# Performance work log

Measured on AMD Instinct MI355X. Metric: run time of the kernel, lower is better.

Reference implementation:

```python
import jax, jax.numpy as jnp
import numpy as np

B, S, E, H = 2, 1024, 4096, 16
D = E // H          # head_dim = 256
RD = 64             # rotary_dim
# Quantization scales (alpha of the int8 GEMM epilogues)
A_QKV = 1.2e-4      # W8A8B8O8 q/k/v projection output scale
A_QK = 2e-4         # BMM_S8T_S8N_F32T alpha (= q_scale * k_scale)
A_PV = 1.0 / 127.0  # BMM_S8T_S8N_S8T alpha (probs quantized by *127)
A_O = 0.01          # W8A8BFP32OFP32 out_proj alpha


def setup_inputs() -> dict:
    key = jax.random.key(0)
    ks = jax.random.split(key, 9)
    ri = lambda k, shp: jax.random.randint(k, shp, -127, 128).astype(jnp.float32)
    return {
        "hidden_states": ri(ks[0], (B, S, E)),   # int8-valued activations
        "Wq": ri(ks[1], (E, E)),
        "Wk": ri(ks[2], (E, E)),
        "Wv": ri(ks[3], (E, E)),
        "Wo": ri(ks[4], (E, E)),
        "bq": ri(ks[5], (E,)),
        "bk": ri(ks[6], (E,)),
        "bv": ri(ks[7], (E,)),
        "bo": jax.random.normal(ks[8], (E,), dtype=jnp.float32) * 0.02,  # fp32 bias
    }


def _linear_i8(x, W, b, alpha):
    # W8A8B8O8Linear: int8 GEMM, scaled, +int8 bias, round+saturate to int8
    y = alpha * (x @ W.T) + b
    return jnp.clip(jnp.round(y), -128, 127)


def _rotate_every_two(x):
    x1 = x[..., ::2]
    x2 = x[..., 1::2]
    return jnp.stack((-x2, x1), axis=-1).reshape(x.shape)


def _apply_rotary(x, sin, cos):
    # duplicate_interleave == repeat each column twice; broadcast over [B, S, H, rd]
    sin = jnp.repeat(sin, 2, axis=-1)[None, :, None, :]
    cos = jnp.repeat(cos, 2, axis=-1)[None, :, None, :]
    r = x * cos + _rotate_every_two(x) * sin
    # torch: clamp(-128,127).to(int8) -> truncate toward zero
    return jnp.trunc(jnp.clip(r, -128.0, 127.0))


def reference(hidden_states, Wq, Wk, Wv, Wo, bq, bk, bv, bo):
    q = _linear_i8(hidden_states, Wq, bq, A_QKV).reshape(B, S, H, D)
    k = _linear_i8(hidden_states, Wk, bk, A_QKV).reshape(B, S, H, D)
    v = _linear_i8(hidden_states, Wv, bv, A_QKV).reshape(B, S, H, D)
    v = v.transpose(0, 2, 1, 3)  # [B, H, S, D]

    # fixed_pos_embedding over rotary_dim
    inv_freq = 1.0 / (10000.0 ** (jnp.arange(0, RD, 2, dtype=jnp.float32) / RD))
    t = jnp.arange(S, dtype=jnp.float32)
    sinusoid = t[:, None] * inv_freq[None, :]   # [S, RD/2]
    sin, cos = jnp.sin(sinusoid), jnp.cos(sinusoid)

    q = jnp.concatenate([_apply_rotary(q[..., :RD], sin, cos), q[..., RD:]], axis=-1)
    k = jnp.concatenate([_apply_rotary(k[..., :RD], sin, cos), k[..., RD:]], axis=-1)
    q = q.transpose(0, 2, 1, 3)  # [B, H, S, D]
    k = k.transpose(0, 2, 1, 3)

    w = A_QK * jnp.einsum('bhqd,bhkd->bhqk', q, k)
    causal = jnp.tril(jnp.ones((S, S), dtype=bool))[None, None]
    w = jnp.where(causal, w, jnp.finfo(jnp.float32).min)
    w = w / jnp.sqrt(jnp.float32(D))  # scale_attn = sqrt(head_dim)
    p = jnp.round(jax.nn.softmax(w, axis=-1) * 127.0)  # int8-valued probs

    # pv_bmm: int8 probs x int8 values -> scaled, round+saturate to int8
    o = jnp.clip(jnp.round(A_PV * jnp.einsum('bhqk,bhkd->bhqd', p, v)), -128, 127)
    o = o.transpose(0, 2, 1, 3).reshape(B, S, E)  # merge heads

    # out_proj: W8A8BFP32OFP32 -> fp32 output
    return A_O * (o @ Wo.T) + bo
```

## Files before the change

### kernel.cpp

```cpp
#include <hip/hip_runtime.h>
#include <hip/hip_bf16.h>

typedef int int32x4 __attribute__((ext_vector_type(4)));
typedef signed char i8;

#define B_ 2
#define S_ 1024
#define E_ 4096
#define H_ 16
#define D_ 256

#define MFMA_I8(a, b, c) __builtin_amdgcn_mfma_i32_16x16x64_i8((a), (b), (c), 0, 0, 0)

__device__ __forceinline__ int32x4 ld16(const void* p) {
    return *reinterpret_cast<const int32x4*>(p);
}

__device__ __forceinline__ void gload16(const void* g, void* l) {
    __builtin_amdgcn_global_load_lds(
        (const __attribute__((address_space(1))) void*)g,
        (__attribute__((address_space(3))) void*)l, 16, 0, 0);
}

#define WAIT_VM3()  asm volatile("s_waitcnt vmcnt(3)" ::: "memory")
#define WAIT_VM0()  asm volatile("s_waitcnt vmcnt(0)" ::: "memory")
#define COMPILER_FENCE() asm volatile("" ::: "memory")

__device__ __forceinline__ int pack4(float4 f) {
    union { int w; i8 b[4]; } u;
    u.b[0] = (i8)f.x; u.b[1] = (i8)f.y; u.b[2] = (i8)f.z; u.b[3] = (i8)f.w;
    return u.w;
}

__global__ void k_f32_to_i8(const float* __restrict__ src, i8* __restrict__ dst, int n4) {
    int i = blockIdx.x * blockDim.x + threadIdx.x;
    if (i >= n4) return;
    reinterpret_cast<int*>(dst)[i] = pack4(reinterpret_cast<const float4*>(src)[i]);
}

__global__ void k_w_to_i8(const float* __restrict__ w0, const float* __restrict__ w1,
                          const float* __restrict__ w2, const float* __restrict__ w3,
                          i8* __restrict__ d0, i8* __restrict__ d1,
                          i8* __restrict__ d2, i8* __restrict__ d3, int n4) {
    int i = blockIdx.x * blockDim.x + threadIdx.x;
    if (i >= n4) return;
    const float* src = (blockIdx.y == 0) ? w0 : (blockIdx.y == 1) ? w1 : (blockIdx.y == 2) ? w2 : w3;
    i8* dst = (blockIdx.y == 0) ? d0 : (blockIdx.y == 1) ? d1 : (blockIdx.y == 2) ? d2 : d3;
    reinterpret_cast<int*>(dst)[i] = pack4(reinterpret_cast<const float4*>(src)[i]);
}

__global__ void k_sincos(float* __restrict__ sin_t, float* __restrict__ cos_t) {
    int idx = blockIdx.x * blockDim.x + threadIdx.x;
    if (idx >= S_ * 32) return;
    int s = idx >> 5, i = idx & 31;
    float ex = (float)(2 * i) / 64.0f;
    float invf = 1.0f / powf(10000.0f, ex);
    float arg = (float)s * invf;
    sin_t[idx] = (float)sin((double)arg);
    cos_t[idx] = (float)cos((double)arg);
}

template<bool OUT_I8>
__device__ __forceinline__ void gemm_core(
    const i8* __restrict__ X, const i8* __restrict__ W, const float* __restrict__ bias,
    void* __restrict__ out, float alpha, int M, int N, int K, i8* lds)
{
    const int nt = K >> 6;
    const int nwg = (M >> 8) * (N >> 7);
    const int q = nwg >> 3;
    const int lin = blockIdx.x;
    const int wg = (lin & 7) * q + (lin >> 3);
    const int nbm = M >> 8;
    const int m0 = (wg % nbm) * 256, n0 = (wg / nbm) * 128;

    const int tid = threadIdx.x, lane = tid & 63, wave = tid >> 6;
    const int wr = wave >> 1, wc = wave & 1, l4 = lane & 15, lh = lane >> 4;

    const int g4 = lh ^ ((l4 >> 1) & 3);
    const int aoff = (wr * 64 + l4) * 64 + g4 * 16;
    const int boff = 16384 + (wc * 64 + l4) * 64 + g4 * 16;

    const int srow = tid >> 2;
    const int sg = (tid & 3) ^ ((tid >> 3) & 3);
    const i8* Asrc = X + (size_t)(m0 + srow) * K + sg * 16;
    const i8* Bsrc = W + (size_t)(n0 + srow) * K + sg * 16;
    const size_t rstep = (size_t)128 * K;
    const int ldst = wave * 1024;

#define BUF(t_) (lds + ((t_) % 3) * 24576)
#define STAGE(t_) do { int kb_ = (t_) * 64; i8* lb_ = BUF(t_);               \
        gload16(Asrc + kb_,         lb_ + ldst);                             \
        gload16(Asrc + rstep + kb_, lb_ + 8192 + ldst);                      \
        gload16(Bsrc + kb_,         lb_ + 16384 + ldst); } while (0)

    int32x4 acc[4][4];
#pragma unroll
    for (int m = 0; m < 4; ++m)
#pragma unroll
        for (int n = 0; n < 4; ++n) acc[m][n] = int32x4{0, 0, 0, 0};

    STAGE(0);
    STAGE(1);

    for (int t = 0; t < nt; ++t) {
        const i8* Tb = BUF(t);
        if (t + 1 < nt) { WAIT_VM3(); } else { WAIT_VM0(); }
        __builtin_amdgcn_s_barrier();
        COMPILER_FENCE();

        if (t + 2 < nt) STAGE(t + 2);

        int32x4 a0, a1, a2, a3, b0, b1, b2, b3;
        a0 = ld16(Tb + aoff);
        b0 = ld16(Tb + boff);        b1 = ld16(Tb + boff + 1024);
        b2 = ld16(Tb + boff + 2048); b3 = ld16(Tb + boff + 3072);
        a1 = ld16(Tb + aoff + 1024);
        a2 = ld16(Tb + aoff + 2048); a3 = ld16(Tb + aoff + 3072);
        __builtin_amdgcn_s_setprio(1);
        acc[0][0] = MFMA_I8(a0, b0, acc[0][0]);
        acc[0][1] = MFMA_I8(a0, b1, acc[0][1]);
        acc[0][2] = MFMA_I8(a0, b2, acc[0][2]);
        acc[0][3] = MFMA_I8(a0, b3, acc[0][3]);
        acc[1][0] = MFMA_I8(a1, b0, acc[1][0]);
        acc[1][1] = MFMA_I8(a1, b1, acc[1][1]);
        acc[1][2] = MFMA_I8(a1, b2, acc[1][2]);
        acc[1][3] = MFMA_I8(a1, b3, acc[1][3]);
        acc[2][0] = MFMA_I8(a2, b0, acc[2][0]);
        acc[2][1] = MFMA_I8(a2, b1, acc[2][1]);
        acc[2][2] = MFMA_I8(a2, b2, acc[2][2]);
        acc[2][3] = MFMA_I8(a2, b3, acc[2][3]);
        acc[3][0] = MFMA_I8(a3, b0, acc[3][0]);
        acc[3][1] = MFMA_I8(a3, b1, acc[3][1]);
        acc[3][2] = MFMA_I8(a3, b2, acc[3][2]);
        acc[3][3] = MFMA_I8(a3, b3, acc[3][3]);
        __builtin_amdgcn_s_setprio(0);
    }
#undef BUF
#undef STAGE

#pragma unroll
    for (int m = 0; m < 4; ++m)
#pragma unroll
        for (int n = 0; n < 4; ++n)
#pragma unroll
            for (int r = 0; r < 4; ++r) {
                int grow = m0 + wr * 64 + m * 16 + lh * 4 + r;
                int gcol = n0 + wc * 64 + n * 16 + l4;
                float y = alpha * (float)acc[m][n][r] + bias[gcol];
                if (OUT_I8) {
                    float v = rintf(y);
                    v = fminf(fmaxf(v, -128.0f), 127.0f);
                    reinterpret_cast<i8*>(out)[(size_t)grow * N + gcol] = (i8)v;
                } else {
                    reinterpret_cast<float*>(out)[(size_t)grow * N + gcol] = y;
                }
            }
}

__global__ __launch_bounds__(512, 4) void k_gemm_qkv(
    const i8* __restrict__ X,
    const i8* __restrict__ w0, const i8* __restrict__ w1, const i8* __restrict__ w2,
    const float* __restrict__ b0, const float* __restrict__ b1, const float* __restrict__ b2,
    i8* __restrict__ o0, i8* __restrict__ o1, i8* __restrict__ o2,
    float alpha, int M, int N, int K)
{
    __shared__ __align__(16) i8 lds[3 * 24576];
    int z = blockIdx.z;
    const i8* W = (z == 0) ? w0 : (z == 1) ? w1 : w2;
    const float* bias = (z == 0) ? b0 : (z == 1) ? b1 : b2;
    i8* out = (z == 0) ? o0 : (z == 1) ? o1 : o2;
    gemm_core<true>(X, W, bias, out, alpha, M, N, K, lds);
}

__global__ __launch_bounds__(512, 4) void k_gemm_out(
    const i8* __restrict__ X, const i8* __restrict__ W, const float* __restrict__ bias,
    float* __restrict__ out, float alpha, int M, int N, int K)
{
    __shared__ __align__(16) i8 lds[3 * 24576];
    gemm_core<false>(X, W, bias, out, alpha, M, N, K, lds);
}

__global__ void k_rope(const i8* __restrict__ qin, const i8* __restrict__ kin,
                       i8* __restrict__ qout, i8* __restrict__ kout,
                       const float* __restrict__ sin_t, const float* __restrict__ cos_t)
{
    const i8* in = blockIdx.y ? kin : qin;
    i8* outp = blockIdx.y ? kout : qout;
    int row = blockIdx.x * 2 + (threadIdx.x >> 7);
    int i = threadIdx.x & 127;
    int b = row / (S_ * H_);
    int s = (row / H_) % S_;
    int h = row % H_;
    const i8* src = in + (size_t)row * D_ + i * 2;
    i8 x1 = src[0], x2 = src[1];
    i8 o1, o2;
    if (i < 32) {
        float c = cos_t[s * 32 + i], sn = sin_t[s * 32 + i];
        float f1 = (float)x1, f2 = (float)x2;
        float r0 = __fadd_rn(__fmul_rn(f1, c), __fmul_rn(-f2, sn));
        float r1 = __fadd_rn(__fmul_rn(f2, c), __fmul_rn(f1, sn));
        r0 = truncf(fminf(fmaxf(r0, -128.0f), 127.0f));
        r1 = truncf(fminf(fmaxf(r1, -128.0f), 127.0f));
        o1 = (i8)r0; o2 = (i8)r1;
    } else { o1 = x1; o2 = x2; }
    size_t ob = ((size_t)(b * H_ + h) * S_ + s) * D_ + i * 2;
    outp[ob] = o1; outp[ob + 1] = o2;
}

__global__ void k_vtrans(const i8* __restrict__ vin, i8* __restrict__ vout) {
    __shared__ int tile[64][17];
    int bh = blockIdx.z;
    int b = bh >> 4, h = bh & 15;
    int s0 = blockIdx.x * 64, d0 = blockIdx.y * 64;
    int t = threadIdx.x;
    {
        int sr = t >> 2, dq = (t & 3) * 16;
        int32x4 v = ld16(vin + ((size_t)(b * S_ + s0 + sr) * H_ + h) * D_ + d0 + dq);
#pragma unroll
        for (int j = 0; j < 4; ++j) tile[sr][dq / 4 + j] = v[j];
    }
    __syncthreads();
    {
        int dr = t >> 2, sq = (t & 3) * 16;
        union { int32x4 v; i8 b[16]; } u;
        const i8* tb = reinterpret_cast<const i8*>(tile);
#pragma unroll
        for (int j = 0; j < 16; ++j) u.b[j] = tb[(sq + j) * 68 + dr];
        *reinterpret_cast<int32x4*>(vout + ((size_t)bh * D_ + d0 + dr) * S_ + s0 + sq) = u.v;
    }
}

struct AttnShared {
    float slx[4][32];
    float r127[32];
    __align__(16) i8 plds[32][80];
};

__device__ __forceinline__ void attn_chunk(int qc, int bh, int tid,
    const i8* __restrict__ Qh, const i8* __restrict__ Kb, const i8* __restrict__ Vb,
    i8* __restrict__ O, AttnShared& sh)
{
    const float C2 = 1.25e-5f * 1.44269504088896f;
    const float APV = 1.0f / 127.0f;
    const int lane = tid & 63, wave = tid >> 6;
    const int l4 = lane & 15, lh = lane >> 4;
    const i8* Qb = Qh + (size_t)(qc * 32) * D_;
    const int nt = (qc * 32 + 31) / 64 + 1;

    int32x4 aq[2][4];
#pragma unroll
    for (int m = 0; m < 2; ++m)
#pragma unroll
        for (int kk = 0; kk < 4; ++kk)
            aq[m][kk] = ld16(Qb + (size_t)(m * 16 + l4) * D_ + kk * 64 + lh * 16);

    float sum_[2][4];
#pragma unroll
    for (int m = 0; m < 2; ++m)
#pragma unroll
        for (int r = 0; r < 4; ++r) sum_[m][r] = 0.0f;

    for (int kt = 0; kt < nt; ++kt) {
        int cb = kt * 64 + wave * 16;
        int32x4 acc0 = int32x4{0,0,0,0}, acc1 = int32x4{0,0,0,0};
#pragma unroll
        for (int kk = 0; kk < 4; ++kk) {
            int32x4 bf = ld16(Kb + (size_t)(cb + l4) * D_ + kk * 64 + lh * 16);
            acc0 = MFMA_I8(aq[0][kk], bf, acc0);
            acc1 = MFMA_I8(aq[1][kk], bf, acc1);
        }
        int gcol = cb + l4;
#pragma unroll
        for (int m = 0; m < 2; ++m) {
            int32x4 accm = m ? acc1 : acc0;
#pragma unroll
            for (int r = 0; r < 4; ++r) {
                int grow = qc * 32 + m * 16 + lh * 4 + r;
                float e = (gcol <= grow) ? exp2f((float)accm[r] * C2) : 0.0f;
                sum_[m][r] += e;
            }
        }
    }

#pragma unroll
    for (int m = 0; m < 2; ++m)
#pragma unroll
        for (int r = 0; r < 4; ++r) {
            float s = sum_[m][r];
            s += __shfl_xor(s, 1);
            s += __shfl_xor(s, 2);
            s += __shfl_xor(s, 4);
            s += __shfl_xor(s, 8);
            if (l4 == 0) sh.slx[wave][m * 16 + lh * 4 + r] = s;
        }
    __syncthreads();
    if (tid < 32)
        sh.r127[tid] = 127.0f /
            (sh.slx[0][tid] + sh.slx[1][tid] + sh.slx[2][tid] + sh.slx[3][tid]);
    __syncthreads();

    int32x4 oacc[2][4];
#pragma unroll
    for (int m = 0; m < 2; ++m)
#pragma unroll
        for (int n = 0; n < 4; ++n) oacc[m][n] = int32x4{0, 0, 0, 0};

    for (int kt = 0; kt < nt; ++kt) {
        int cb = kt * 64 + wave * 16;
        int32x4 acc0 = int32x4{0,0,0,0}, acc1 = int32x4{0,0,0,0};
#pragma unroll
        for (int kk = 0; kk < 4; ++kk) {
            int32x4 bf = ld16(Kb + (size_t)(cb + l4) * D_ + kk * 64 + lh * 16);
            acc0 = MFMA_I8(aq[0][kk], bf, acc0);
            acc1 = MFMA_I8(aq[1][kk], bf, acc1);
        }
        int gcol = cb + l4;
        i8 pv[2][4];
#pragma unroll
        for (int m = 0; m < 2; ++m) {
            int32x4 accm = m ? acc1 : acc0;
#pragma unroll
            for (int r = 0; r < 4; ++r) {
                int rowi = m * 16 + lh * 4 + r;
                int grow = qc * 32 + rowi;
                float e = (gcol <= grow) ? exp2f((float)accm[r] * C2) : 0.0f;
                pv[m][r] = (i8)(int)rintf(e * sh.r127[rowi]);
            }
        }
        __syncthreads();
#pragma unroll
        for (int m = 0; m < 2; ++m)
#pragma unroll
            for (int r = 0; r < 4; ++r)
                sh.plds[m * 16 + lh * 4 + r][wave * 16 + l4] = pv[m][r];
        __syncthreads();
        int32x4 a0 = ld16(&sh.plds[l4][lh * 16]);
        int32x4 a1 = ld16(&sh.plds[16 + l4][lh * 16]);
#pragma unroll
        for (int n = 0; n < 4; ++n) {
            int32x4 bf = ld16(Vb + (size_t)(wave * 64 + n * 16 + l4) * S_ + kt * 64 + lh * 16);
            oacc[0][n] = MFMA_I8(a0, bf, oacc[0][n]);
            oacc[1][n] = MFMA_I8(a1, bf, oacc[1][n]);
        }
    }

    int b = bh >> 4, h = bh & 15;
#pragma unroll
    for (int m = 0; m < 2; ++m)
#pragma unroll
        for (int r = 0; r < 4; ++r) {
            int s = qc * 32 + m * 16 + lh * 4 + r;
#pragma unroll
            for (int n = 0; n < 4; ++n) {
                float o = rintf(APV * (float)oacc[m][n][r]);
                o = fminf(fmaxf(o, -128.0f), 127.0f);
                O[((size_t)(b * S_ + s) * H_ + h) * D_ + wave * 64 + n * 16 + l4] = (i8)o;
            }
        }
}

__global__ __launch_bounds__(256) void k_attn(const i8* __restrict__ Q, const i8* __restrict__ K,
                                              const i8* __restrict__ V, i8* __restrict__ O)
{
    __shared__ AttnShared sh;
    int bh = blockIdx.x;
    int p = blockIdx.y;
    int tid = threadIdx.x;
    const i8* Qh = Q + (size_t)bh * S_ * D_;
    const i8* Kb = K + (size_t)bh * S_ * D_;
    const i8* Vb = V + (size_t)bh * D_ * S_;
    attn_chunk((S_ / 32 - 1) - p, bh, tid, Qh, Kb, Vb, O, sh);
    attn_chunk(p, bh, tid, Qh, Kb, Vb, O, sh);
}

extern "C" void kernel_launch(void* const* d_in, const int* in_sizes, int n_in,
                              void* d_out, int out_size, void* d_ws, size_t ws_size,
                              hipStream_t stream) {
    const float* hs = (const float*)d_in[0];
    const float* Wq = (const float*)d_in[1];
    const float* Wk = (const float*)d_in[2];
    const float* Wv = (const float*)d_in[3];
    const float* Wo = (const float*)d_in[4];
    const float* bq = (const float*)d_in[5];
    const float* bk = (const float*)d_in[6];
    const float* bv = (const float*)d_in[7];
    const float* bo = (const float*)d_in[8];
    float* out = (float*)d_out;

    size_t off = 0;
    char* wsb = (char*)d_ws;
    auto carve = [&](size_t bytes) { char* p = wsb + off; off += (bytes + 255) & ~(size_t)255; return p; };
    const size_t ME = (size_t)B_ * S_ * E_;
    const size_t EE = (size_t)E_ * E_;
    i8* x8  = (i8*)carve(ME);
    i8* wq8 = (i8*)carve(EE);
    i8* wk8 = (i8*)carve(EE);
    i8* wv8 = (i8*)carve(EE);
    i8* wo8 = (i8*)carve(EE);
    i8* q8  = (i8*)carve(ME);
    i8* k8  = (i8*)carve(ME);
    i8* v8  = (i8*)carve(ME);
    i8* qr  = (i8*)carve(ME);
    i8* kr  = (i8*)carve(ME);
    i8* vt  = (i8*)carve(ME);
    i8* o8  = (i8*)carve(ME);
    float* sin_t = (float*)carve((size_t)S_ * 32 * 4);
    float* cos_t = (float*)carve((size_t)S_ * 32 * 4);

    int n4_me = (int)(ME / 4), n4_ee = (int)(EE / 4);
    k_f32_to_i8<<<(n4_me + 255) / 256, 256, 0, stream>>>(hs, x8, n4_me);
    k_w_to_i8<<<dim3((n4_ee + 255) / 256, 4), 256, 0, stream>>>(
        Wq, Wk, Wv, Wo, wq8, wk8, wv8, wo8, n4_ee);
    k_sincos<<<(S_ * 32 + 255) / 256, 256, 0, stream>>>(sin_t, cos_t);

    const int M = B_ * S_, N = E_, Kd = E_;
    const int nwg = (M / 256) * (N / 128);
    k_gemm_qkv<<<dim3(nwg, 1, 3), 512, 0, stream>>>(
        x8, wq8, wk8, wv8, bq, bk, bv, q8, k8, v8, 0.00012f, M, N, Kd);

    k_rope<<<dim3((B_ * S_ * H_) / 2, 2), 256, 0, stream>>>(q8, k8, qr, kr, sin_t, cos_t);
    k_vtrans<<<dim3(S_ / 64, D_ / 64, B_ * H_), 256, 0, stream>>>(v8, vt);
    k_attn<<<dim3(B_ * H_, S_ / 64), 256, 0, stream>>>(qr, kr, vt, o8);

    k_gemm_out<<<nwg, 512, 0, stream>>>(o8, wo8, bo, out, 0.01f, M, N, Kd);
}
```

Measured before the change: 299.9 us.

## Load GEMM A operand directly into registers, stage only B through LDS

The int8 GEMM core stops staging the activation (A) tile through LDS. Each wave now loads its own A fragments straight from global memory into a register double buffer, one K-tile ahead, and the loop is unrolled by two to swap the buffers. Only the weight (B) tile still goes through the triple-buffered LDS ring, so LDS per block drops from 72 KB to 24 KB, which should allow more resident blocks and removes the A-side LDS reads. The cost is that waves sharing the same A rows now fetch them separately from global memory, and global latency is hidden by only one tile of prefetch. The unroll by two also assumes an even number of K-tiles.

After: 501.5 us. 1.67x slower.

```diff
diff --git a/kernel.cpp b/kernel.cpp
--- a/kernel.cpp
+++ b/kernel.cpp
@@ -22,7 +22,7 @@
         (__attribute__((address_space(3))) void*)l, 16, 0, 0);
 }
 
-#define WAIT_VM3()  asm volatile("s_waitcnt vmcnt(3)" ::: "memory")
+#define WAIT_VM1()  asm volatile("s_waitcnt vmcnt(1)" ::: "memory")
 #define WAIT_VM0()  asm volatile("s_waitcnt vmcnt(0)" ::: "memory")
 #define COMPILER_FENCE() asm volatile("" ::: "memory")
 
@@ -77,21 +77,17 @@
     const int wr = wave >> 1, wc = wave & 1, l4 = lane & 15, lh = lane >> 4;
 
     const int g4 = lh ^ ((l4 >> 1) & 3);
-    const int aoff = (wr * 64 + l4) * 64 + g4 * 16;
-    const int boff = 16384 + (wc * 64 + l4) * 64 + g4 * 16;
+    const int boff = (wc * 64 + l4) * 64 + g4 * 16;
 
     const int srow = tid >> 2;
     const int sg = (tid & 3) ^ ((tid >> 3) & 3);
-    const i8* Asrc = X + (size_t)(m0 + srow) * K + sg * 16;
     const i8* Bsrc = W + (size_t)(n0 + srow) * K + sg * 16;
-    const size_t rstep = (size_t)128 * K;
     const int ldst = wave * 1024;
 
-#define BUF(t_) (lds + ((t_) % 3) * 24576)
-#define STAGE(t_) do { int kb_ = (t_) * 64; i8* lb_ = BUF(t_);               \
-        gload16(Asrc + kb_,         lb_ + ldst);                             \
-        gload16(Asrc + rstep + kb_, lb_ + 8192 + ldst);                      \
-        gload16(Bsrc + kb_,         lb_ + 16384 + ldst); } while (0)
+    const i8* Aglb = X + (size_t)(m0 + wr * 64 + l4) * K + lh * 16;
+    const size_t fstep = (size_t)16 * K;
+
+#define STAGE_B(t_) gload16(Bsrc + (t_) * 64, lds + ((t_) % 3) * 8192 + ldst)
 
     int32x4 acc[4][4];
 #pragma unroll
@@ -99,44 +95,57 @@
 #pragma unroll
         for (int n = 0; n < 4; ++n) acc[m][n] = int32x4{0, 0, 0, 0};
 
-    STAGE(0);
-    STAGE(1);
-
-    for (int t = 0; t < nt; ++t) {
-        const i8* Tb = BUF(t);
-        if (t + 1 < nt) { WAIT_VM3(); } else { WAIT_VM0(); }
-        __builtin_amdgcn_s_barrier();
-        COMPILER_FENCE();
-
-        if (t + 2 < nt) STAGE(t + 2);
-
-        int32x4 a0, a1, a2, a3, b0, b1, b2, b3;
-        a0 = ld16(Tb + aoff);
-        b0 = ld16(Tb + boff);        b1 = ld16(Tb + boff + 1024);
-        b2 = ld16(Tb + boff + 2048); b3 = ld16(Tb + boff + 3072);
-        a1 = ld16(Tb + aoff + 1024);
-        a2 = ld16(Tb + aoff + 2048); a3 = ld16(Tb + aoff + 3072);
-        __builtin_amdgcn_s_setprio(1);
-        acc[0][0] = MFMA_I8(a0, b0, acc[0][0]);
-        acc[0][1] = MFMA_I8(a0, b1, acc[0][1]);
-        acc[0][2] = MFMA_I8(a0, b2, acc[0][2]);
-        acc[0][3] = MFMA_I8(a0, b3, acc[0][3]);
-        acc[1][0] = MFMA_I8(a1, b0, acc[1][0]);
-        acc[1][1] = MFMA_I8(a1, b1, acc[1][1]);
-        acc[1][2] = MFMA_I8(a1, b2, acc[1][2]);
-        acc[1][3] = MFMA_I8(a1, b3, acc[1][3]);
-        acc[2][0] = MFMA_I8(a2, b0, acc[2][0]);
-        acc[2][1] = MFMA_I8(a2, b1, acc[2][1]);
-        acc[2][2] = MFMA_I8(a2, b2, acc[2][2]);
-        acc[2][3] = MFMA_I8(a2, b3, acc[2][3]);
-        acc[3][0] = MFMA_I8(a3, b0, acc[3][0]);
-        acc[3][1] = MFMA_I8(a3, b1, acc[3][1]);
-        acc[3][2] = MFMA_I8(a3, b2, acc[3][2]);
-        acc[3][3] = MFMA_I8(a3, b3, acc[3][3]);
-        __builtin_amdgcn_s_setprio(0);
-    }
-#undef BUF
-#undef STAGE
+    int32x4 aR0[4], aR1[4];
+
+    {
+        const i8* ap = Aglb;
+        aR0[0] = ld16(ap);             aR0[1] = ld16(ap + fstep);
+        aR0[2] = ld16(ap + 2 * fstep); aR0[3] = ld16(ap + 3 * fstep);
+    }
+    STAGE_B(0);
+    STAGE_B(1);
+
+#define TILE_BODY(t_, AC, AN) do {                                            \
+        if ((t_) + 1 < nt) { WAIT_VM1(); } else { WAIT_VM0(); }               \
+        __builtin_amdgcn_s_barrier();                                         \
+        COMPILER_FENCE();                                                     \
+        if ((t_) + 1 < nt) {                                                  \
+            const i8* ap_ = Aglb + ((t_) + 1) * 64;                           \
+            AN[0] = ld16(ap_);             AN[1] = ld16(ap_ + fstep);         \
+            AN[2] = ld16(ap_ + 2 * fstep); AN[3] = ld16(ap_ + 3 * fstep);     \
+        }                                                                     \
+        if ((t_) + 2 < nt) STAGE_B((t_) + 2);                                 \
+        {                                                                     \
+            const i8* Tb_ = lds + ((t_) % 3) * 8192;                          \
+            int32x4 b0 = ld16(Tb_ + boff);        int32x4 b1 = ld16(Tb_ + boff + 1024); \
+            int32x4 b2 = ld16(Tb_ + boff + 2048); int32x4 b3 = ld16(Tb_ + boff + 3072); \
+            __builtin_amdgcn_s_setprio(1);                                    \
+            acc[0][0] = MFMA_I8(AC[0], b0, acc[0][0]);                        \
+            acc[0][1] = MFMA_I8(AC[0], b1, acc[0][1]);                        \
+            acc[0][2] = MFMA_I8(AC[0], b2, acc[0][2]);                        \
+            acc[0][3] = MFMA_I8(AC[0], b3, acc[0][3]);                        \
+            acc[1][0] = MFMA_I8(AC[1], b0, acc[1][0]);                        \
+            acc[1][1] = MFMA_I8(AC[1], b1, acc[1][1]);                        \
+            acc[1][2] = MFMA_I8(AC[1], b2, acc[1][2]);                        \
+            acc[1][3] = MFMA_I8(AC[1], b3, acc[1][3]);                        \
+            acc[2][0] = MFMA_I8(AC[2], b0, acc[2][0]);                        \
+            acc[2][1] = MFMA_I8(AC[2], b1, acc[2][1]);                        \
+            acc[2][2] = MFMA_I8(AC[2], b2, acc[2][2]);                        \
+            acc[2][3] = MFMA_I8(AC[2], b3, acc[2][3]);                        \
+            acc[3][0] = MFMA_I8(AC[3], b0, acc[3][0]);                        \
+            acc[3][1] = MFMA_I8(AC[3], b1, acc[3][1]);                        \
+            acc[3][2] = MFMA_I8(AC[3], b2, acc[3][2]);                        \
+            acc[3][3] = MFMA_I8(AC[3], b3, acc[3][3]);                        \
+            __builtin_amdgcn_s_setprio(0);                                    \
+        }                                                                     \
+    } while (0)
+
+    for (int tt = 0; tt < nt; tt += 2) {
+        TILE_BODY(tt, aR0, aR1);
+        TILE_BODY(tt + 1, aR1, aR0);
+    }
+#undef TILE_BODY
+#undef STAGE_B
 
 #pragma unroll
     for (int m = 0; m < 4; ++m)
@@ -164,7 +173,7 @@
     i8* __restrict__ o0, i8* __restrict__ o1, i8* __restrict__ o2,
     float alpha, int M, int N, int K)
 {
-    __shared__ __align__(16) i8 lds[3 * 24576];
+    __shared__ __align__(16) i8 lds[3 * 8192];
     int z = blockIdx.z;
     const i8* W = (z == 0) ? w0 : (z == 1) ? w1 : w2;
     const float* bias = (z == 0) ? b0 : (z == 1) ? b1 : b2;
@@ -176,7 +185,7 @@
     const i8* __restrict__ X, const i8* __restrict__ W, const float* __restrict__ bias,
     float* __restrict__ out, float alpha, int M, int N, int K)
 {
-    __shared__ __align__(16) i8 lds[3 * 24576];
+    __shared__ __align__(16) i8 lds[3 * 8192];
     gemm_core<false>(X, W, bias, out, alpha, M, N, K, lds);
 }
 
```

## Use ping-pong double-buffered 8-phase pipeline for QKV int8 GEMM

Applied to the files above, without the earlier changes.

Replaces the triple-buffered QKV GEMM main loop with a double-buffered schedule that splits each k-tile into half-tile phases, interleaving LDS reads, global-to-LDS prefetches of individual A/B halves, and MFMA bursts separated by barriers. LDS use drops from three buffers to two, which could allow more resident workgroups, and global loads are spread more finely across compute phases. The cost is many more barriers per iteration and tighter waitcnt dependencies, which could stall waves if load latency is not hidden. The output projection GEMM keeps the old path.

After: 316.3 us. 5.5% more time.

```diff
diff --git a/kernel.cpp b/kernel.cpp
--- a/kernel.cpp
+++ b/kernel.cpp
@@ -23,7 +23,10 @@
 }
 
 #define WAIT_VM3()  asm volatile("s_waitcnt vmcnt(3)" ::: "memory")
+#define WAIT_VM1()  asm volatile("s_waitcnt vmcnt(1)" ::: "memory")
 #define WAIT_VM0()  asm volatile("s_waitcnt vmcnt(0)" ::: "memory")
+#define WAIT_LGKM0() do { asm volatile("s_waitcnt lgkmcnt(0)" ::: "memory"); \
+                          __builtin_amdgcn_sched_barrier(0); } while (0)
 #define COMPILER_FENCE() asm volatile("" ::: "memory")
 
 __device__ __forceinline__ int pack4(float4 f) {
@@ -87,8 +90,8 @@
     const size_t rstep = (size_t)128 * K;
     const int ldst = wave * 1024;
 
-#define BUF(t_) (lds + ((t_) % 3) * 24576)
-#define STAGE(t_) do { int kb_ = (t_) * 64; i8* lb_ = BUF(t_);               \
+#define BUF3(t_) (lds + ((t_) % 3) * 24576)
+#define STAGE3(t_) do { int kb_ = (t_) * 64; i8* lb_ = BUF3(t_);             \
         gload16(Asrc + kb_,         lb_ + ldst);                             \
         gload16(Asrc + rstep + kb_, lb_ + 8192 + ldst);                      \
         gload16(Bsrc + kb_,         lb_ + 16384 + ldst); } while (0)
@@ -99,16 +102,16 @@
 #pragma unroll
         for (int n = 0; n < 4; ++n) acc[m][n] = int32x4{0, 0, 0, 0};
 
-    STAGE(0);
-    STAGE(1);
+    STAGE3(0);
+    STAGE3(1);
 
     for (int t = 0; t < nt; ++t) {
-        const i8* Tb = BUF(t);
+        const i8* Tb = BUF3(t);
         if (t + 1 < nt) { WAIT_VM3(); } else { WAIT_VM0(); }
         __builtin_amdgcn_s_barrier();
         COMPILER_FENCE();
 
-        if (t + 2 < nt) STAGE(t + 2);
+        if (t + 2 < nt) STAGE3(t + 2);
 
         int32x4 a0, a1, a2, a3, b0, b1, b2, b3;
         a0 = ld16(Tb + aoff);
@@ -135,8 +138,8 @@
         acc[3][3] = MFMA_I8(a3, b3, acc[3][3]);
         __builtin_amdgcn_s_setprio(0);
     }
-#undef BUF
-#undef STAGE
+#undef BUF3
+#undef STAGE3
 
 #pragma unroll
     for (int m = 0; m < 4; ++m)
@@ -157,6 +160,144 @@
             }
 }
 
+__device__ __forceinline__ void gemm8p_core(
+    const i8* __restrict__ X, const i8* __restrict__ W, const float* __restrict__ bias,
+    i8* __restrict__ out, float alpha, int M, int N, int K, i8* lds)
+{
+    const int nt = K >> 6;
+    const int nwg = (M >> 8) * (N >> 7);
+    const int q = nwg >> 3;
+    const int lin = blockIdx.x;
+    const int wg = (lin & 7) * q + (lin >> 3);
+    const int nbm = M >> 8;
+    const int m0 = (wg % nbm) * 256, n0 = (wg / nbm) * 128;
+
+    const int tid = threadIdx.x, lane = tid & 63, wave = tid >> 6;
+    const int wr = wave >> 1, wc = wave & 1, l4 = lane & 15, lh = lane >> 4;
+
+    const int g4 = lh ^ ((l4 >> 1) & 3);
+    const int aoff = (wr * 64 + l4) * 64 + g4 * 16;
+    const int boff = 16384 + (wc * 64 + l4) * 64 + g4 * 16;
+
+    const int srow = tid >> 2;
+    const int sg = (tid & 3) ^ ((tid >> 3) & 3);
+    const i8* Asrc = X + (size_t)(m0 + srow) * K + sg * 16;
+    const i8* Bsrc = W + (size_t)(n0 + srow) * K + sg * 16;
+    const size_t hstep = (size_t)128 * K;
+    const int ldst = wave * 1024;
+
+#define BUF8(t_) (lds + ((t_) & 1) * 24576)
+#define SA8(t_, h_) gload16(Asrc + (h_) * hstep + (t_) * 64, \
+                            BUF8(t_) + (h_) * 8192 + ldst)
+#define SB8(t_)     gload16(Bsrc + (t_) * 64, BUF8(t_) + 16384 + ldst)
+
+    int32x4 acc[4][4];
+#pragma unroll
+    for (int m = 0; m < 4; ++m)
+#pragma unroll
+        for (int n = 0; n < 4; ++n) acc[m][n] = int32x4{0, 0, 0, 0};
+
+    SA8(0, 0); SA8(0, 1); SB8(0);
+    WAIT_VM0();
+    SB8(1);
+    __builtin_amdgcn_s_barrier();
+    COMPILER_FENCE();
+
+    for (int t0 = 0; t0 < nt; t0 += 2) {
+        const int t1 = t0 + 1;
+        const bool full = (t0 + 2 < nt);
+        const i8* Tb0 = BUF8(t0);
+        const i8* Tb1 = BUF8(t1);
+        int32x4 a0, a1, b0, b1, b2, b3;
+
+        b0 = ld16(Tb0 + boff);        b1 = ld16(Tb0 + boff + 1024);
+        b2 = ld16(Tb0 + boff + 2048); b3 = ld16(Tb0 + boff + 3072);
+        a0 = ld16(Tb0 + aoff);        a1 = ld16(Tb0 + aoff + 1024);
+        SA8(t1, 0);
+        __builtin_amdgcn_s_barrier();
+        WAIT_LGKM0();
+        __builtin_amdgcn_s_setprio(1);
+        acc[0][0] = MFMA_I8(a0, b0, acc[0][0]);
+        acc[0][1] = MFMA_I8(a0, b1, acc[0][1]);
+        acc[0][2] = MFMA_I8(a0, b2, acc[0][2]);
+        acc[0][3] = MFMA_I8(a0, b3, acc[0][3]);
+        acc[1][0] = MFMA_I8(a1, b0, acc[1][0]);
+        acc[1][1] = MFMA_I8(a1, b1, acc[1][1]);
+        acc[1][2] = MFMA_I8(a1, b2, acc[1][2]);
+        acc[1][3] = MFMA_I8(a1, b3, acc[1][3]);
+        __builtin_amdgcn_s_setprio(0);
+        __builtin_amdgcn_s_barrier();
+
+        a0 = ld16(Tb0 + aoff + 2048); a1 = ld16(Tb0 + aoff + 3072);
+        SA8(t1, 1);
+        if (full) { SB8(t0 + 2); WAIT_VM1(); } else { WAIT_VM0(); }
+        __builtin_amdgcn_s_barrier();
+        WAIT_LGKM0();
+        __builtin_amdgcn_s_setprio(1);
+        acc[2][0] = MFMA_I8(a0, b0, acc[2][0]);
+        acc[2][1] = MFMA_I8(a0, b1, acc[2][1]);
+        acc[2][2] = MFMA_I8(a0, b2, acc[2][2]);
+        acc[2][3] = MFMA_I8(a0, b3, acc[2][3]);
+        acc[3][0] = MFMA_I8(a1, b0, acc[3][0]);
+        acc[3][1] = MFMA_I8(a1, b1, acc[3][1]);
+        acc[3][2] = MFMA_I8(a1, b2, acc[3][2]);
+        acc[3][3] = MFMA_I8(a1, b3, acc[3][3]);
+        __builtin_amdgcn_s_setprio(0);
+        __builtin_amdgcn_s_barrier();
+
+        b0 = ld16(Tb1 + boff);        b1 = ld16(Tb1 + boff + 1024);
+        b2 = ld16(Tb1 + boff + 2048); b3 = ld16(Tb1 + boff + 3072);
+        a0 = ld16(Tb1 + aoff);        a1 = ld16(Tb1 + aoff + 1024);
+        if (full) SA8(t0 + 2, 0);
+        __builtin_amdgcn_s_barrier();
+        WAIT_LGKM0();
+        __builtin_amdgcn_s_setprio(1);
+        acc[0][0] = MFMA_I8(a0, b0, acc[0][0]);
+        acc[0][1] = MFMA_I8(a0, b1, acc[0][1]);
+        acc[0][2] = MFMA_I8(a0, b2, acc[0][2]);
+        acc[0][3] = MFMA_I8(a0, b3, acc[0][3]);
+        acc[1][0] = MFMA_I8(a1, b0, acc[1][0]);
+        acc[1][1] = MFMA_I8(a1, b1, acc[1][1]);
+        acc[1][2] = MFMA_I8(a1, b2, acc[1][2]);
+        acc[1][3] = MFMA_I8(a1, b3, acc[1][3]);
+        __builtin_amdgcn_s_setprio(0);
+        __builtin_amdgcn_s_barrier();
+
+        a0 = ld16(Tb1 + aoff + 2048); a1 = ld16(Tb1 + aoff + 3072);
+        if (full) { SA8(t0 + 2, 1); SB8(t1 + 2); WAIT_VM1(); } else { WAIT_VM0(); }
+        __builtin_amdgcn_s_barrier();
+        WAIT_LGKM0();
+        __builtin_amdgcn_s_setprio(1);
+        acc[2][0] = MFMA_I8(a0, b0, acc[2][0]);
+        acc[2][1] = MFMA_I8(a0, b1, acc[2][1]);
+        acc[2][2] = MFMA_I8(a0, b2, acc[2][2]);
+        acc[2][3] = MFMA_I8(a0, b3, acc[2][3]);
+        acc[3][0] = MFMA_I8(a1, b0, acc[3][0]);
+        acc[3][1] = MFMA_I8(a1, b1, acc[3][1]);
+        acc[3][2] = MFMA_I8(a1, b2, acc[3][2]);
+        acc[3][3] = MFMA_I8(a1, b3, acc[3][3]);
+        __builtin_amdgcn_s_setprio(0);
+        __builtin_amdgcn_s_barrier();
+    }
+#undef BUF8
+#undef SA8
+#undef SB8
+
+#pragma unroll
+    for (int m = 0; m < 4; ++m)
+#pragma unroll
+        for (int n = 0; n < 4; ++n)
+#pragma unroll
+            for (int r = 0; r < 4; ++r) {
+                int grow = m0 + wr * 64 + m * 16 + lh * 4 + r;
+                int gcol = n0 + wc * 64 + n * 16 + l4;
+                float y = alpha * (float)acc[m][n][r] + bias[gcol];
+                float v = rintf(y);
+                v = fminf(fmaxf(v, -128.0f), 127.0f);
+                out[(size_t)grow * N + gcol] = (i8)v;
+            }
+}
+
 __global__ __launch_bounds__(512, 4) void k_gemm_qkv(
     const i8* __restrict__ X,
     const i8* __restrict__ w0, const i8* __restrict__ w1, const i8* __restrict__ w2,
@@ -164,12 +305,12 @@
     i8* __restrict__ o0, i8* __restrict__ o1, i8* __restrict__ o2,
     float alpha, int M, int N, int K)
 {
-    __shared__ __align__(16) i8 lds[3 * 24576];
+    __shared__ __align__(16) i8 lds[2 * 24576];
     int z = blockIdx.z;
     const i8* W = (z == 0) ? w0 : (z == 1) ? w1 : w2;
     const float* bias = (z == 0) ? b0 : (z == 1) ? b1 : b2;
     i8* out = (z == 0) ? o0 : (z == 1) ? o1 : o2;
-    gemm_core<true>(X, W, bias, out, alpha, M, N, K, lds);
+    gemm8p_core(X, W, bias, out, alpha, M, N, K, lds);
 }
 
 __global__ __launch_bounds__(512, 4) void k_gemm_out(
```
